# Performance work log

Hardware: AMD Instinct MI355X
Metric: run time of the kernel (lower is better)

The kernel has to match this reference:

```python
import jax, jax.numpy as jnp
import numpy as np

L, D, K = 1024, 256, 1
B, N = 16, 4096
EPS = 1e-5
NEG = -1e9


def _leaky(v):
    return jnp.where(v >= 0, v, 0.2 * v)


def setup_inputs() -> dict:
    key = jax.random.key(0)
    ks = jax.random.split(key, 16)
    s = 0.02
    x = jax.random.normal(ks[0], (B, N, L), dtype=jnp.float32)
    mask = jax.random.randint(ks[1], (B, N), 0, 2, dtype=jnp.int32)
    # guarantee >=1 valid patch per slide
    mask = mask.at[:, 0].set(1)
    return {
        "x": x,
        "mask": mask,
        # attention MLP: Linear(L,D) -> BN(D) -> LeakyReLU -> Linear(D,D) -> LeakyReLU -> Linear(D,K)
        "W1": jax.random.normal(ks[2], (L, D), jnp.float32) * s,
        "b1": jnp.zeros((D,), jnp.float32),
        "bn_gamma": jnp.ones((D,), jnp.float32),
        "bn_beta": jnp.zeros((D,), jnp.float32),
        "bn_mean": jax.random.normal(ks[3], (D,), jnp.float32) * 0.1,
        "bn_var": jax.random.uniform(ks[4], (D,), jnp.float32, 0.5, 1.5),
        "W2": jax.random.normal(ks[5], (D, D), jnp.float32) * s,
        "b2": jnp.zeros((D,), jnp.float32),
        "W3": jax.random.normal(ks[6], (D, K), jnp.float32) * s,
        "b3": jnp.zeros((K,), jnp.float32),
        # classifier MLP: Linear(L,D) -> ReLU -> Linear(D,D) -> ReLU -> Linear(D,2)
        "C1": jax.random.normal(ks[7], (L, D), jnp.float32) * s,
        "c1": jnp.zeros((D,), jnp.float32),
        "C2": jax.random.normal(ks[8], (D, D), jnp.float32) * s,
        "c2": jnp.zeros((D,), jnp.float32),
        "C3": jax.random.normal(ks[9], (D, 2), jnp.float32) * s,
        "c3": jnp.zeros((2,), jnp.float32),
    }


def reference(x, mask, W1, b1, bn_gamma, bn_beta, bn_mean, bn_var,
              W2, b2, W3, b3, C1, c1, C2, c2, C3, c3):
    # attention scores for every patch (batched; invalid patches masked later)
    h = jnp.einsum('bnl,ld->bnd', x, W1) + b1                     # [B,N,D]
    h = (h - bn_mean) * jax.lax.rsqrt(bn_var + EPS) * bn_gamma + bn_beta  # eval-mode BN
    h = _leaky(h)
    h = _leaky(jnp.einsum('bnd,de->bne', h, W2) + b2)             # [B,N,D]
    scores = (jnp.einsum('bnd,dk->bnk', h, W3) + b3)[..., 0]      # [B,N] (K=1)
    # masked softmax over patches == softmax over gathered valid patches
    valid = mask.astype(bool)
    A = jax.nn.softmax(jnp.where(valid, scores, NEG), axis=1)     # [B,N]
    M = jnp.einsum('bn,bnl->bl', A, x)                            # [B,L] attention pool
    # classifier
    z = jax.nn.relu(M @ C1 + c1)
    z = jax.nn.relu(z @ C2 + c2)
    logits = z @ C3 + c3                                          # [B,2]
    Y_prob = jax.nn.softmax(logits, axis=1)
    Y_hat = jnp.argmax(Y_prob, axis=1)
    return Y_prob, Y_hat
```

## Files before the change

### kernel.cpp

```cpp
#include <hip/hip_runtime.h>

#define BB 16
#define NN 4096
#define LL 1024
#define DD 256
#define MTOT (BB*NN)
#define EPSV 1e-5f
#define NEGV -1e9f

typedef float f32x4_t __attribute__((ext_vector_type(4)));
typedef short bf16x8_t __attribute__((ext_vector_type(8)));

#define MFMA16(a, b, c) __builtin_amdgcn_mfma_f32_16x16x32_bf16((a), (b), (c), 0, 0, 0)

__device__ __forceinline__ ushort f2bf(float f) {
    unsigned u = __builtin_bit_cast(unsigned, f);
    u += 0x7fffu + ((u >> 16) & 1u);
    return (ushort)(u >> 16);
}
__device__ __forceinline__ float bf2f(ushort u) {
    unsigned v = ((unsigned)u) << 16;
    return __builtin_bit_cast(float, v);
}
__device__ __forceinline__ void split1(float f, ushort& hi, ushort& lo) {
    hi = f2bf(f);
    lo = f2bf(f - bf2f(hi));
}
__device__ __forceinline__ float leaky(float v) { return v >= 0.f ? v : 0.2f * v; }

__global__ __launch_bounds__(256) void prep_split_w1(const float* __restrict__ W1,
                                                     ushort* __restrict__ thi,
                                                     ushort* __restrict__ tlo) {
    int idx = blockIdx.x * 256 + threadIdx.x;
    int k = idx >> 8, d = idx & 255;
    float v = W1[idx];
    ushort hi, lo; split1(v, hi, lo);
    thi[d * 1024 + k] = hi;
    tlo[d * 1024 + k] = lo;
}

__global__ __launch_bounds__(256) void prep_split_w2(const float* __restrict__ W2,
                                                     ushort* __restrict__ thi,
                                                     ushort* __restrict__ tlo) {
    int idx = blockIdx.x * 256 + threadIdx.x;
    int k = idx >> 8, d = idx & 255;
    float v = W2[idx];
    ushort hi, lo; split1(v, hi, lo);
    thi[d * 256 + k] = hi;
    tlo[d * 256 + k] = lo;
}

__global__ __launch_bounds__(256) void prep_bn(const float* __restrict__ g,
                                               const float* __restrict__ beta,
                                               const float* __restrict__ mean,
                                               const float* __restrict__ var,
                                               float* __restrict__ scale,
                                               float* __restrict__ shift) {
    int d = threadIdx.x;
    float s = g[d] * rsqrtf(var[d] + EPSV);
    scale[d] = s;
    shift[d] = beta[d] - mean[d] * s;
}

__global__ __launch_bounds__(256) void zero_scores(float* __restrict__ s) {
    s[blockIdx.x * 256 + threadIdx.x] = 0.f;
}

__global__ __launch_bounds__(256, 2) void gemm1_kernel(const float* __restrict__ x,
                                                       const ushort* __restrict__ Bhi,
                                                       const ushort* __restrict__ Blo,
                                                       const float* __restrict__ b1,
                                                       const float* __restrict__ scale,
                                                       const float* __restrict__ shift,
                                                       float* __restrict__ h) {
    __shared__ ushort sAhi[128 * 64];
    __shared__ ushort sAlo[128 * 64];
    __shared__ ushort sBhi[128 * 64];
    __shared__ ushort sBlo[128 * 64];

    const int tid = threadIdx.x;
    const int lane = tid & 63;
    const int wave = tid >> 6;
    const int wm = wave >> 1, wn = wave & 1;
    const int mblk = blockIdx.x, nblk = blockIdx.y;

    f32x4_t acc[4][4] = {};

    const int ar = tid >> 4;
    const int ac = (tid & 15) * 4;
    const int brr = tid >> 3;
    const int bcc = (tid & 7) * 8;

    const size_t xbase = (size_t)(mblk * 128) * 1024;
    const int dbase = nblk * 128;

    for (int k0 = 0; k0 < 1024; k0 += 64) {
        #pragma unroll
        for (int s = 0; s < 8; ++s) {
            int r = s * 16 + ar;
            float4 v = *reinterpret_cast<const float4*>(x + xbase + (size_t)r * 1024 + k0 + ac);
            int uo = r * 64 + (ac ^ ((r & 7) << 3));
            ushort4 hi, lo;
            split1(v.x, hi.x, lo.x); split1(v.y, hi.y, lo.y);
            split1(v.z, hi.z, lo.z); split1(v.w, hi.w, lo.w);
            *reinterpret_cast<ushort4*>(&sAhi[uo]) = hi;
            *reinterpret_cast<ushort4*>(&sAlo[uo]) = lo;
        }
        #pragma unroll
        for (int s = 0; s < 4; ++s) {
            int r = s * 32 + brr;
            size_t gsrc = (size_t)(dbase + r) * 1024 + k0 + bcc;
            int uo = r * 64 + (bcc ^ ((r & 7) << 3));
            *reinterpret_cast<uint4*>(&sBhi[uo]) = *reinterpret_cast<const uint4*>(Bhi + gsrc);
            *reinterpret_cast<uint4*>(&sBlo[uo]) = *reinterpret_cast<const uint4*>(Blo + gsrc);
        }
        __syncthreads();
        #pragma unroll
        for (int s = 0; s < 2; ++s) {
            const int kb = s * 32 + (lane >> 4) * 8;
            bf16x8_t aHi[4], aLo[4], bHi[4], bLo[4];
            #pragma unroll
            for (int i = 0; i < 4; ++i) {
                int row = wm * 64 + i * 16 + (lane & 15);
                int uo = row * 64 + (kb ^ ((row & 7) << 3));
                aHi[i] = *reinterpret_cast<const bf16x8_t*>(&sAhi[uo]);
                aLo[i] = *reinterpret_cast<const bf16x8_t*>(&sAlo[uo]);
            }
            #pragma unroll
            for (int j = 0; j < 4; ++j) {
                int col = wn * 64 + j * 16 + (lane & 15);
                int uo = col * 64 + (kb ^ ((col & 7) << 3));
                bHi[j] = *reinterpret_cast<const bf16x8_t*>(&sBhi[uo]);
                bLo[j] = *reinterpret_cast<const bf16x8_t*>(&sBlo[uo]);
            }
            #pragma unroll
            for (int i = 0; i < 4; ++i)
                #pragma unroll
                for (int j = 0; j < 4; ++j) {
                    acc[i][j] = MFMA16(aHi[i], bHi[j], acc[i][j]);
                    acc[i][j] = MFMA16(aHi[i], bLo[j], acc[i][j]);
                    acc[i][j] = MFMA16(aLo[i], bHi[j], acc[i][j]);
                }
        }
        __syncthreads();
    }
    #pragma unroll
    for (int j = 0; j < 4; ++j) {
        int col = dbase + wn * 64 + j * 16 + (lane & 15);
        float bj = b1[col], sc = scale[col], sh = shift[col];
        #pragma unroll
        for (int i = 0; i < 4; ++i) {
            int row0 = mblk * 128 + wm * 64 + i * 16 + ((lane >> 4) << 2);
            #pragma unroll
            for (int r = 0; r < 4; ++r) {
                float v = acc[i][j][r] + bj;
                v = v * sc + sh;
                h[(size_t)(row0 + r) * 256 + col] = leaky(v);
            }
        }
    }
}

__global__ __launch_bounds__(256, 2) void gemm2_kernel(const float* __restrict__ h,
                                                       const ushort* __restrict__ Bhi,
                                                       const ushort* __restrict__ Blo,
                                                       const float* __restrict__ b2,
                                                       const float* __restrict__ W3,
                                                       float* __restrict__ scores) {
    __shared__ ushort sAhi[128 * 64];
    __shared__ ushort sAlo[128 * 64];
    __shared__ ushort sBhi[128 * 64];
    __shared__ ushort sBlo[128 * 64];

    const int tid = threadIdx.x;
    const int lane = tid & 63;
    const int wave = tid >> 6;
    const int wm = wave >> 1, wn = wave & 1;
    const int mblk = blockIdx.x, nblk = blockIdx.y;

    f32x4_t acc[4][4] = {};

    const int ar = tid >> 4;
    const int ac = (tid & 15) * 4;
    const int brr = tid >> 3;
    const int bcc = (tid & 7) * 8;

    const size_t hbase = (size_t)(mblk * 128) * 256;
    const int dbase = nblk * 128;

    for (int k0 = 0; k0 < 256; k0 += 64) {
        #pragma unroll
        for (int s = 0; s < 8; ++s) {
            int r = s * 16 + ar;
            float4 v = *reinterpret_cast<const float4*>(h + hbase + (size_t)r * 256 + k0 + ac);
            int uo = r * 64 + (ac ^ ((r & 7) << 3));
            ushort4 hi, lo;
            split1(v.x, hi.x, lo.x); split1(v.y, hi.y, lo.y);
            split1(v.z, hi.z, lo.z); split1(v.w, hi.w, lo.w);
            *reinterpret_cast<ushort4*>(&sAhi[uo]) = hi;
            *reinterpret_cast<ushort4*>(&sAlo[uo]) = lo;
        }
        #pragma unroll
        for (int s = 0; s < 4; ++s) {
            int r = s * 32 + brr;
            size_t gsrc = (size_t)(dbase + r) * 256 + k0 + bcc;
            int uo = r * 64 + (bcc ^ ((r & 7) << 3));
            *reinterpret_cast<uint4*>(&sBhi[uo]) = *reinterpret_cast<const uint4*>(Bhi + gsrc);
            *reinterpret_cast<uint4*>(&sBlo[uo]) = *reinterpret_cast<const uint4*>(Blo + gsrc);
        }
        __syncthreads();
        #pragma unroll
        for (int s = 0; s < 2; ++s) {
            const int kb = s * 32 + (lane >> 4) * 8;
            bf16x8_t aHi[4], aLo[4], bHi[4], bLo[4];
            #pragma unroll
            for (int i = 0; i < 4; ++i) {
                int row = wm * 64 + i * 16 + (lane & 15);
                int uo = row * 64 + (kb ^ ((row & 7) << 3));
                aHi[i] = *reinterpret_cast<const bf16x8_t*>(&sAhi[uo]);
                aLo[i] = *reinterpret_cast<const bf16x8_t*>(&sAlo[uo]);
            }
            #pragma unroll
            for (int j = 0; j < 4; ++j) {
                int col = wn * 64 + j * 16 + (lane & 15);
                int uo = col * 64 + (kb ^ ((col & 7) << 3));
                bHi[j] = *reinterpret_cast<const bf16x8_t*>(&sBhi[uo]);
                bLo[j] = *reinterpret_cast<const bf16x8_t*>(&sBlo[uo]);
            }
            #pragma unroll
            for (int i = 0; i < 4; ++i)
                #pragma unroll
                for (int j = 0; j < 4; ++j) {
                    acc[i][j] = MFMA16(aHi[i], bHi[j], acc[i][j]);
                    acc[i][j] = MFMA16(aHi[i], bLo[j], acc[i][j]);
                    acc[i][j] = MFMA16(aLo[i], bHi[j], acc[i][j]);
                }
        }
        __syncthreads();
    }
    #pragma unroll
    for (int i = 0; i < 4; ++i) {
        float rowsum[4] = {0.f, 0.f, 0.f, 0.f};
        #pragma unroll
        for (int j = 0; j < 4; ++j) {
            int col = dbase + wn * 64 + j * 16 + (lane & 15);
            float bj = b2[col];
            float w3v = W3[col];
            #pragma unroll
            for (int r = 0; r < 4; ++r) {
                float v = leaky(acc[i][j][r] + bj);
                rowsum[r] += v * w3v;
            }
        }
        int row0 = mblk * 128 + wm * 64 + i * 16 + ((lane >> 4) << 2);
        #pragma unroll
        for (int r = 0; r < 4; ++r) {
            float s = rowsum[r];
            s += __shfl_xor(s, 1);
            s += __shfl_xor(s, 2);
            s += __shfl_xor(s, 4);
            s += __shfl_xor(s, 8);
            if ((lane & 15) == 0) atomicAdd(&scores[row0 + r], s);
        }
    }
}

__global__ __launch_bounds__(256) void softmax_kernel(const float* __restrict__ scores,
                                                      const int* __restrict__ mask,
                                                      const float* __restrict__ b3,
                                                      float* __restrict__ A,
                                                      float* __restrict__ Mz) {
    int b = blockIdx.x, tid = threadIdx.x;
    __shared__ float red[8];
    float loc[16];
    float mx = -3.4e38f;
    float b3v = b3[0];
    #pragma unroll
    for (int j = 0; j < 16; ++j) {
        int n = j * 256 + tid;
        float s = scores[b * 4096 + n] + b3v;
        if (mask[b * 4096 + n] == 0) s = NEGV;
        loc[j] = s;
        mx = fmaxf(mx, s);
    }
    #pragma unroll
    for (int o = 1; o < 64; o <<= 1) mx = fmaxf(mx, __shfl_xor(mx, o));
    if ((tid & 63) == 0) red[tid >> 6] = mx;
    __syncthreads();
    mx = fmaxf(fmaxf(red[0], red[1]), fmaxf(red[2], red[3]));
    float sum = 0.f;
    #pragma unroll
    for (int j = 0; j < 16; ++j) {
        loc[j] = expf(loc[j] - mx);
        sum += loc[j];
    }
    #pragma unroll
    for (int o = 1; o < 64; o <<= 1) sum += __shfl_xor(sum, o);
    if ((tid & 63) == 0) red[4 + (tid >> 6)] = sum;
    __syncthreads();
    sum = red[4] + red[5] + red[6] + red[7];
    float inv = 1.0f / sum;
    #pragma unroll
    for (int j = 0; j < 16; ++j) A[b * 4096 + j * 256 + tid] = loc[j] * inv;
    #pragma unroll
    for (int j = 0; j < 4; ++j) Mz[b * 1024 + j * 256 + tid] = 0.f;
}

__global__ __launch_bounds__(256) void pool_kernel(const float* __restrict__ x,
                                                   const float* __restrict__ A,
                                                   float* __restrict__ M) {
    int b = blockIdx.x, s = blockIdx.y, tid = threadIdx.x;
    __shared__ float sA[64];
    if (tid < 64) sA[tid] = A[b * 4096 + s * 64 + tid];
    __syncthreads();
    float4 acc = {0.f, 0.f, 0.f, 0.f};
    const float* xp = x + ((size_t)b * 4096 + (size_t)s * 64) * 1024 + tid * 4;
    #pragma unroll 4
    for (int n = 0; n < 64; ++n) {
        float a = sA[n];
        float4 v = *reinterpret_cast<const float4*>(xp + (size_t)n * 1024);
        acc.x += a * v.x; acc.y += a * v.y; acc.z += a * v.z; acc.w += a * v.w;
    }
    float* mp = M + b * 1024 + tid * 4;
    atomicAdd(mp + 0, acc.x);
    atomicAdd(mp + 1, acc.y);
    atomicAdd(mp + 2, acc.z);
    atomicAdd(mp + 3, acc.w);
}

__global__ __launch_bounds__(256) void classifier_kernel(const float* __restrict__ M,
                                                         const float* __restrict__ C1,
                                                         const float* __restrict__ c1,
                                                         const float* __restrict__ C2,
                                                         const float* __restrict__ c2,
                                                         const float* __restrict__ C3,
                                                         const float* __restrict__ c3,
                                                         float* __restrict__ out) {
    int b = blockIdx.x, tid = threadIdx.x;
    __shared__ float sM[1024];
    __shared__ float sZ[256];
    __shared__ float sZ2[256];
    __shared__ float sLg[2];
    #pragma unroll
    for (int j = 0; j < 4; ++j) sM[j * 256 + tid] = M[b * 1024 + j * 256 + tid];
    __syncthreads();
    float a = c1[tid];
    for (int l = 0; l < 1024; ++l) a += sM[l] * C1[l * 256 + tid];
    sZ[tid] = a > 0.f ? a : 0.f;
    __syncthreads();
    float a2 = c2[tid];
    for (int l = 0; l < 256; ++l) a2 += sZ[l] * C2[l * 256 + tid];
    sZ2[tid] = a2 > 0.f ? a2 : 0.f;
    __syncthreads();
    if (tid < 2) {
        float lg = c3[tid];
        for (int l = 0; l < 256; ++l) lg += sZ2[l] * C3[l * 2 + tid];
        sLg[tid] = lg;
    }
    __syncthreads();
    if (tid == 0) {
        float l0 = sLg[0], l1 = sLg[1];
        float mxv = fmaxf(l0, l1);
        float e0 = expf(l0 - mxv), e1 = expf(l1 - mxv);
        float sm = e0 + e1;
        out[b * 2 + 0] = e0 / sm;
        out[b * 2 + 1] = e1 / sm;
        out[32 + b] = (l1 > l0) ? 1.f : 0.f;
    }
}

extern "C" void kernel_launch(void* const* d_in, const int* in_sizes, int n_in,
                              void* d_out, int out_size, void* d_ws, size_t ws_size,
                              hipStream_t stream) {
    const float* x        = (const float*)d_in[0];
    const int*   mask     = (const int*)d_in[1];
    const float* W1       = (const float*)d_in[2];
    const float* b1       = (const float*)d_in[3];
    const float* bn_gamma = (const float*)d_in[4];
    const float* bn_beta  = (const float*)d_in[5];
    const float* bn_mean  = (const float*)d_in[6];
    const float* bn_var   = (const float*)d_in[7];
    const float* W2       = (const float*)d_in[8];
    const float* b2       = (const float*)d_in[9];
    const float* W3       = (const float*)d_in[10];
    const float* b3       = (const float*)d_in[11];
    const float* C1       = (const float*)d_in[12];
    const float* c1       = (const float*)d_in[13];
    const float* C2       = (const float*)d_in[14];
    const float* c2       = (const float*)d_in[15];
    const float* C3       = (const float*)d_in[16];
    const float* c3       = (const float*)d_in[17];
    float* out = (float*)d_out;

    ushort* w1t_hi  = (ushort*)d_ws;
    ushort* w1t_lo  = w1t_hi + 262144;
    ushort* w2t_hi  = w1t_lo + 262144;
    ushort* w2t_lo  = w2t_hi + 65536;
    float*  bn_scale = (float*)(w2t_lo + 65536);
    float*  bn_shift = bn_scale + 256;
    float*  scores   = bn_shift + 256;
    float*  attnA    = scores + 65536;
    float*  Mpool    = attnA + 65536;
    float*  h        = Mpool + 16384;

    prep_split_w1<<<1024, 256, 0, stream>>>(W1, w1t_hi, w1t_lo);
    prep_split_w2<<<256, 256, 0, stream>>>(W2, w2t_hi, w2t_lo);
    prep_bn<<<1, 256, 0, stream>>>(bn_gamma, bn_beta, bn_mean, bn_var, bn_scale, bn_shift);
    zero_scores<<<256, 256, 0, stream>>>(scores);

    gemm1_kernel<<<dim3(512, 2), 256, 0, stream>>>(x, w1t_hi, w1t_lo, b1, bn_scale, bn_shift, h);
    gemm2_kernel<<<dim3(512, 2), 256, 0, stream>>>(h, w2t_hi, w2t_lo, b2, W3, scores);
    softmax_kernel<<<16, 256, 0, stream>>>(scores, mask, b3, attnA, Mpool);
    pool_kernel<<<dim3(16, 64), 256, 0, stream>>>(x, attnA, Mpool);
    classifier_kernel<<<16, 256, 0, stream>>>(Mpool, C1, c1, C2, c2, C3, c3, out);
}
```

Before: 637.9 us.

## Pre-tile weights and h into interleaved hi/lo bf16 tiles with direct LDS loads

```diff
diff --git a/kernel.cpp b/kernel.cpp
--- a/kernel.cpp
+++ b/kernel.cpp
@@ -1,12 +1,8 @@
 #include <hip/hip_runtime.h>
 
-#define BB 16
-#define NN 4096
-#define LL 1024
-#define DD 256
-#define MTOT (BB*NN)
 #define EPSV 1e-5f
 #define NEGV -1e9f
+#define XRS(r) (((r)&7)<<3)
 
 typedef float f32x4_t __attribute__((ext_vector_type(4)));
 typedef short bf16x8_t __attribute__((ext_vector_type(8)));
@@ -28,234 +24,202 @@
 }
 __device__ __forceinline__ float leaky(float v) { return v >= 0.f ? v : 0.2f * v; }
 
-__global__ __launch_bounds__(256) void prep_split_w1(const float* __restrict__ W1,
-                                                     ushort* __restrict__ thi,
-                                                     ushort* __restrict__ tlo) {
-    int idx = blockIdx.x * 256 + threadIdx.x;
-    int k = idx >> 8, d = idx & 255;
-    float v = W1[idx];
-    ushort hi, lo; split1(v, hi, lo);
-    thi[d * 1024 + k] = hi;
-    tlo[d * 1024 + k] = lo;
-}
-
-__global__ __launch_bounds__(256) void prep_split_w2(const float* __restrict__ W2,
-                                                     ushort* __restrict__ thi,
-                                                     ushort* __restrict__ tlo) {
-    int idx = blockIdx.x * 256 + threadIdx.x;
-    int k = idx >> 8, d = idx & 255;
-    float v = W2[idx];
-    ushort hi, lo; split1(v, hi, lo);
-    thi[d * 256 + k] = hi;
-    tlo[d * 256 + k] = lo;
-}
-
-__global__ __launch_bounds__(256) void prep_bn(const float* __restrict__ g,
-                                               const float* __restrict__ beta,
-                                               const float* __restrict__ mean,
-                                               const float* __restrict__ var,
-                                               float* __restrict__ scale,
-                                               float* __restrict__ shift) {
-    int d = threadIdx.x;
-    float s = g[d] * rsqrtf(var[d] + EPSV);
-    scale[d] = s;
-    shift[d] = beta[d] - mean[d] * s;
-}
-
-__global__ __launch_bounds__(256) void zero_scores(float* __restrict__ s) {
-    s[blockIdx.x * 256 + threadIdx.x] = 0.f;
-}
-
-__global__ __launch_bounds__(256, 2) void gemm1_kernel(const float* __restrict__ x,
-                                                       const ushort* __restrict__ Bhi,
-                                                       const ushort* __restrict__ Blo,
+__device__ __forceinline__ void g2lds16(void* lds, const void* g) {
+    __builtin_amdgcn_global_load_lds(
+        (const __attribute__((address_space(1))) void*)g,
+        (__attribute__((address_space(3))) void*)lds, 16, 0, 0);
+}
+
+__global__ __launch_bounds__(256) void prep_all(const float* __restrict__ W1,
+                                                const float* __restrict__ W2,
+                                                const float* __restrict__ g,
+                                                const float* __restrict__ be,
+                                                const float* __restrict__ mn,
+                                                const float* __restrict__ vr,
+                                                ushort* __restrict__ w1t,
+                                                ushort* __restrict__ w2t,
+                                                float* __restrict__ bnsc,
+                                                float* __restrict__ bnsh,
+                                                float* __restrict__ scores) {
+    int blk = blockIdx.x, tid = threadIdx.x;
+    if (blk < 1024) {
+        int idx = blk * 256 + tid;
+        int k = idx >> 8, d = idx & 255;
+        ushort hi, lo; split1(W1[idx], hi, lo);
+        int u = (k >> 5) * 16384 + d * 64 + ((k & 31) ^ XRS(d));
+        w1t[u] = hi; w1t[u ^ 32] = lo;
+    } else if (blk < 1280) {
+        int idx = (blk - 1024) * 256 + tid;
+        int k = idx >> 8, e = idx & 255;
+        ushort hi, lo; split1(W2[idx], hi, lo);
+        int u = (k >> 5) * 16384 + e * 64 + ((k & 31) ^ XRS(e));
+        w2t[u] = hi; w2t[u ^ 32] = lo;
+    } else if (blk == 1280) {
+        float s = g[tid] * rsqrtf(vr[tid] + EPSV);
+        bnsc[tid] = s; bnsh[tid] = be[tid] - mn[tid] * s;
+    } else {
+        int idx = (blk - 1281) * 256 + tid;
+        scores[idx] = 0.f;
+    }
+}
+
+__global__ __launch_bounds__(256, 4) void gemm1_kernel(const float* __restrict__ x,
+                                                       const ushort* __restrict__ w1t,
                                                        const float* __restrict__ b1,
-                                                       const float* __restrict__ scale,
-                                                       const float* __restrict__ shift,
-                                                       float* __restrict__ h) {
-    __shared__ ushort sAhi[128 * 64];
-    __shared__ ushort sAlo[128 * 64];
-    __shared__ ushort sBhi[128 * 64];
-    __shared__ ushort sBlo[128 * 64];
-
-    const int tid = threadIdx.x;
-    const int lane = tid & 63;
-    const int wave = tid >> 6;
+                                                       const float* __restrict__ bnsc,
+                                                       const float* __restrict__ bnsh,
+                                                       ushort* __restrict__ hsp) {
+    __shared__ ushort sA[128 * 64];
+    __shared__ ushort sB[128 * 64];
+
+    const int bid = blockIdx.x;
+    const int swz = (bid & 7) * 128 + (bid >> 3);
+    const int mblk = swz >> 1, nblk = swz & 1;
+    const int tid = threadIdx.x, lane = tid & 63, wave = tid >> 6;
     const int wm = wave >> 1, wn = wave & 1;
-    const int mblk = blockIdx.x, nblk = blockIdx.y;
 
     f32x4_t acc[4][4] = {};
 
-    const int ar = tid >> 4;
-    const int ac = (tid & 15) * 4;
-    const int brr = tid >> 3;
-    const int bcc = (tid & 7) * 8;
-
+    const int arow = tid >> 3;
+    const int acol = (tid & 7) * 4;
     const size_t xbase = (size_t)(mblk * 128) * 1024;
-    const int dbase = nblk * 128;
-
-    for (int k0 = 0; k0 < 1024; k0 += 64) {
-        #pragma unroll
-        for (int s = 0; s < 8; ++s) {
-            int r = s * 16 + ar;
-            float4 v = *reinterpret_cast<const float4*>(x + xbase + (size_t)r * 1024 + k0 + ac);
-            int uo = r * 64 + (ac ^ ((r & 7) << 3));
+    const ushort* wbase = w1t + nblk * 8192;
+
+    for (int k0 = 0; k0 < 32; ++k0) {
+        const ushort* bs = wbase + (size_t)k0 * 16384;
+        #pragma unroll
+        for (int i = 0; i < 4; ++i)
+            g2lds16(&sB[i * 2048 + tid * 8], bs + i * 2048 + tid * 8);
+        #pragma unroll
+        for (int s = 0; s < 4; ++s) {
+            int r = s * 32 + arow;
+            float4 v = *reinterpret_cast<const float4*>(x + xbase + (size_t)r * 1024 + k0 * 32 + acol);
             ushort4 hi, lo;
             split1(v.x, hi.x, lo.x); split1(v.y, hi.y, lo.y);
             split1(v.z, hi.z, lo.z); split1(v.w, hi.w, lo.w);
-            *reinterpret_cast<ushort4*>(&sAhi[uo]) = hi;
-            *reinterpret_cast<ushort4*>(&sAlo[uo]) = lo;
-        }
-        #pragma unroll
-        for (int s = 0; s < 4; ++s) {
-            int r = s * 32 + brr;
-            size_t gsrc = (size_t)(dbase + r) * 1024 + k0 + bcc;
-            int uo = r * 64 + (bcc ^ ((r & 7) << 3));
-            *reinterpret_cast<uint4*>(&sBhi[uo]) = *reinterpret_cast<const uint4*>(Bhi + gsrc);
-            *reinterpret_cast<uint4*>(&sBlo[uo]) = *reinterpret_cast<const uint4*>(Blo + gsrc);
+            int u = r * 64 + (acol ^ XRS(r));
+            *reinterpret_cast<ushort4*>(&sA[u]) = hi;
+            *reinterpret_cast<ushort4*>(&sA[u ^ 32]) = lo;
         }
         __syncthreads();
-        #pragma unroll
-        for (int s = 0; s < 2; ++s) {
-            const int kb = s * 32 + (lane >> 4) * 8;
-            bf16x8_t aHi[4], aLo[4], bHi[4], bLo[4];
+        {
+            const int g8 = (lane >> 4) * 8;
+            bf16x8_t aH[4], aL[4], bH[4], bL[4];
             #pragma unroll
             for (int i = 0; i < 4; ++i) {
                 int row = wm * 64 + i * 16 + (lane & 15);
-                int uo = row * 64 + (kb ^ ((row & 7) << 3));
-                aHi[i] = *reinterpret_cast<const bf16x8_t*>(&sAhi[uo]);
-                aLo[i] = *reinterpret_cast<const bf16x8_t*>(&sAlo[uo]);
+                int u = row * 64 + (g8 ^ XRS(row));
+                aH[i] = *reinterpret_cast<const bf16x8_t*>(&sA[u]);
+                aL[i] = *reinterpret_cast<const bf16x8_t*>(&sA[u ^ 32]);
             }
             #pragma unroll
             for (int j = 0; j < 4; ++j) {
                 int col = wn * 64 + j * 16 + (lane & 15);
-                int uo = col * 64 + (kb ^ ((col & 7) << 3));
-                bHi[j] = *reinterpret_cast<const bf16x8_t*>(&sBhi[uo]);
-                bLo[j] = *reinterpret_cast<const bf16x8_t*>(&sBlo[uo]);
+                int u = col * 64 + (g8 ^ XRS(col));
+                bH[j] = *reinterpret_cast<const bf16x8_t*>(&sB[u]);
+                bL[j] = *reinterpret_cast<const bf16x8_t*>(&sB[u ^ 32]);
             }
             #pragma unroll
             for (int i = 0; i < 4; ++i)
                 #pragma unroll
                 for (int j = 0; j < 4; ++j) {
-                    acc[i][j] = MFMA16(aHi[i], bHi[j], acc[i][j]);
-                    acc[i][j] = MFMA16(aHi[i], bLo[j], acc[i][j]);
-                    acc[i][j] = MFMA16(aLo[i], bHi[j], acc[i][j]);
+                    acc[i][j] = MFMA16(aH[i], bH[j], acc[i][j]);
+                    acc[i][j] = MFMA16(aH[i], bL[j], acc[i][j]);
+                    acc[i][j] = MFMA16(aL[i], bH[j], acc[i][j]);
                 }
         }
         __syncthreads();
     }
     #pragma unroll
     for (int j = 0; j < 4; ++j) {
-        int col = dbase + wn * 64 + j * 16 + (lane & 15);
-        float bj = b1[col], sc = scale[col], sh = shift[col];
+        int colg = nblk * 128 + wn * 64 + j * 16 + (lane & 15);
+        float bj = b1[colg], sc = bnsc[colg], sh = bnsh[colg];
+        int cl = colg & 31;
+        size_t tbase = ((size_t)mblk * 8 + (colg >> 5)) * 8192;
         #pragma unroll
         for (int i = 0; i < 4; ++i) {
-            int row0 = mblk * 128 + wm * 64 + i * 16 + ((lane >> 4) << 2);
+            int rl0 = wm * 64 + i * 16 + ((lane >> 4) << 2);
             #pragma unroll
             for (int r = 0; r < 4; ++r) {
-                float v = acc[i][j][r] + bj;
-                v = v * sc + sh;
-                h[(size_t)(row0 + r) * 256 + col] = leaky(v);
-            }
-        }
-    }
-}
-
-__global__ __launch_bounds__(256, 2) void gemm2_kernel(const float* __restrict__ h,
-                                                       const ushort* __restrict__ Bhi,
-                                                       const ushort* __restrict__ Blo,
+                int rl = rl0 + r;
+                float v = leaky((acc[i][j][r] + bj) * sc + sh);
+                ushort hi, lo; split1(v, hi, lo);
+                int u = rl * 64 + (cl ^ XRS(rl));
+                hsp[tbase + u] = hi;
+                hsp[tbase + (u ^ 32)] = lo;
+            }
+        }
+    }
+}
+
+__global__ __launch_bounds__(256, 4) void gemm2_kernel(const ushort* __restrict__ hsp,
+                                                       const ushort* __restrict__ w2t,
                                                        const float* __restrict__ b2,
                                                        const float* __restrict__ W3,
                                                        float* __restrict__ scores) {
-    __shared__ ushort sAhi[128 * 64];
-    __shared__ ushort sAlo[128 * 64];
-    __shared__ ushort sBhi[128 * 64];
-    __shared__ ushort sBlo[128 * 64];
-
-    const int tid = threadIdx.x;
-    const int lane = tid & 63;
-    const int wave = tid >> 6;
+    __shared__ ushort sA[128 * 64];
+    __shared__ ushort sB[128 * 64];
+
+    const int bid = blockIdx.x;
+    const int swz = (bid & 7) * 128 + (bid >> 3);
+    const int mblk = swz >> 1, nblk = swz & 1;
+    const int tid = threadIdx.x, lane = tid & 63, wave = tid >> 6;
     const int wm = wave >> 1, wn = wave & 1;
-    const int mblk = blockIdx.x, nblk = blockIdx.y;
 
     f32x4_t acc[4][4] = {};
 
-    const int ar = tid >> 4;
-    const int ac = (tid & 15) * 4;
-    const int brr = tid >> 3;
-    const int bcc = (tid & 7) * 8;
-
-    const size_t hbase = (size_t)(mblk * 128) * 256;
-    const int dbase = nblk * 128;
-
-    for (int k0 = 0; k0 < 256; k0 += 64) {
-        #pragma unroll
-        for (int s = 0; s < 8; ++s) {
-            int r = s * 16 + ar;
-            float4 v = *reinterpret_cast<const float4*>(h + hbase + (size_t)r * 256 + k0 + ac);
-            int uo = r * 64 + (ac ^ ((r & 7) << 3));
-            ushort4 hi, lo;
-            split1(v.x, hi.x, lo.x); split1(v.y, hi.y, lo.y);
-            split1(v.z, hi.z, lo.z); split1(v.w, hi.w, lo.w);
-            *reinterpret_cast<ushort4*>(&sAhi[uo]) = hi;
-            *reinterpret_cast<ushort4*>(&sAlo[uo]) = lo;
-        }
-        #pragma unroll
-        for (int s = 0; s < 4; ++s) {
-            int r = s * 32 + brr;
-            size_t gsrc = (size_t)(dbase + r) * 256 + k0 + bcc;
-            int uo = r * 64 + (bcc ^ ((r & 7) << 3));
-            *reinterpret_cast<uint4*>(&sBhi[uo]) = *reinterpret_cast<const uint4*>(Bhi + gsrc);
-            *reinterpret_cast<uint4*>(&sBlo[uo]) = *reinterpret_cast<const uint4*>(Blo + gsrc);
+    for (int k0 = 0; k0 < 8; ++k0) {
+        const ushort* as = hsp + ((size_t)mblk * 8 + k0) * 8192;
+        const ushort* bs = w2t + (size_t)k0 * 16384 + nblk * 8192;
+        #pragma unroll
+        for (int i = 0; i < 4; ++i) {
+            g2lds16(&sA[i * 2048 + tid * 8], as + i * 2048 + tid * 8);
+            g2lds16(&sB[i * 2048 + tid * 8], bs + i * 2048 + tid * 8);
         }
         __syncthreads();
-        #pragma unroll
-        for (int s = 0; s < 2; ++s) {
-            const int kb = s * 32 + (lane >> 4) * 8;
-            bf16x8_t aHi[4], aLo[4], bHi[4], bLo[4];
+        {
+            const int g8 = (lane >> 4) * 8;
+            bf16x8_t aH[4], aL[4], bH[4], bL[4];
             #pragma unroll
             for (int i = 0; i < 4; ++i) {
                 int row = wm * 64 + i * 16 + (lane & 15);
-                int uo = row * 64 + (kb ^ ((row & 7) << 3));
-                aHi[i] = *reinterpret_cast<const bf16x8_t*>(&sAhi[uo]);
-                aLo[i] = *reinterpret_cast<const bf16x8_t*>(&sAlo[uo]);
+                int u = row * 64 + (g8 ^ XRS(row));
+                aH[i] = *reinterpret_cast<const bf16x8_t*>(&sA[u]);
+                aL[i] = *reinterpret_cast<const bf16x8_t*>(&sA[u ^ 32]);
             }
             #pragma unroll
             for (int j = 0; j < 4; ++j) {
                 int col = wn * 64 + j * 16 + (lane & 15);
-                int uo = col * 64 + (kb ^ ((col & 7) << 3));
-                bHi[j] = *reinterpret_cast<const bf16x8_t*>(&sBhi[uo]);
-                bLo[j] = *reinterpret_cast<const bf16x8_t*>(&sBlo[uo]);
+                int u = col * 64 + (g8 ^ XRS(col));
+                bH[j] = *reinterpret_cast<const bf16x8_t*>(&sB[u]);
+                bL[j] = *reinterpret_cast<const bf16x8_t*>(&sB[u ^ 32]);
             }
             #pragma unroll
             for (int i = 0; i < 4; ++i)
                 #pragma unroll
                 for (int j = 0; j < 4; ++j) {
-                    acc[i][j] = MFMA16(aHi[i], bHi[j], acc[i][j]);
-                    acc[i][j] = MFMA16(aHi[i], bLo[j], acc[i][j]);
-                    acc[i][j] = MFMA16(aLo[i], bHi[j], acc[i][j]);
+                    acc[i][j] = MFMA16(aH[i], bH[j], acc[i][j]);
+                    acc[i][j] = MFMA16(aH[i], bL[j], acc[i][j]);
+                    acc[i][j] = MFMA16(aL[i], bH[j], acc[i][j]);
                 }
         }
         __syncthreads();
     }
     #pragma unroll
     for (int i = 0; i < 4; ++i) {
-        float rowsum[4] = {0.f, 0.f, 0.f, 0.f};
+        float rs[4] = {0.f, 0.f, 0.f, 0.f};
         #pragma unroll
         for (int j = 0; j < 4; ++j) {
-            int col = dbase + wn * 64 + j * 16 + (lane & 15);
-            float bj = b2[col];
-            float w3v = W3[col];
-            #pragma unroll
-            for (int r = 0; r < 4; ++r) {
-                float v = leaky(acc[i][j][r] + bj);
-                rowsum[r] += v * w3v;
-            }
+            int colg = nblk * 128 + wn * 64 + j * 16 + (lane & 15);
+            float bj = b2[colg], w3v = W3[colg];
+            #pragma unroll
+            for (int r = 0; r < 4; ++r)
+                rs[r] += leaky(acc[i][j][r] + bj) * w3v;
         }
         int row0 = mblk * 128 + wm * 64 + i * 16 + ((lane >> 4) << 2);
         #pragma unroll
         for (int r = 0; r < 4; ++r) {
-            float s = rowsum[r];
+            float s = rs[r];
             s += __shfl_xor(s, 1);
             s += __shfl_xor(s, 2);
             s += __shfl_xor(s, 4);
@@ -310,13 +274,13 @@
                                                    const float* __restrict__ A,
                                                    float* __restrict__ M) {
     int b = blockIdx.x, s = blockIdx.y, tid = threadIdx.x;
-    __shared__ float sA[64];
-    if (tid < 64) sA[tid] = A[b * 4096 + s * 64 + tid];
+    __shared__ float sA[128];
+    if (tid < 128) sA[tid] = A[b * 4096 + s * 128 + tid];
     __syncthreads();
     float4 acc = {0.f, 0.f, 0.f, 0.f};
-    const float* xp = x + ((size_t)b * 4096 + (size_t)s * 64) * 1024 + tid * 4;
-    #pragma unroll 4
-    for (int n = 0; n < 64; ++n) {
+    const float* xp = x + ((size_t)b * 4096 + (size_t)s * 128) * 1024 + tid * 4;
+    #pragma unroll 8
+    for (int n = 0; n < 128; ++n) {
         float a = sA[n];
         float4 v = *reinterpret_cast<const float4*>(xp + (size_t)n * 1024);
         acc.x += a * v.x; acc.y += a * v.y; acc.z += a * v.z; acc.w += a * v.w;
@@ -392,25 +356,20 @@
     const float* c3       = (const float*)d_in[17];
     float* out = (float*)d_out;
 
-    ushort* w1t_hi  = (ushort*)d_ws;
-    ushort* w1t_lo  = w1t_hi + 262144;
-    ushort* w2t_hi  = w1t_lo + 262144;
-    ushort* w2t_lo  = w2t_hi + 65536;
-    float*  bn_scale = (float*)(w2t_lo + 65536);
-    float*  bn_shift = bn_scale + 256;
-    float*  scores   = bn_shift + 256;
-    float*  attnA    = scores + 65536;
-    float*  Mpool    = attnA + 65536;
-    float*  h        = Mpool + 16384;
-
-    prep_split_w1<<<1024, 256, 0, stream>>>(W1, w1t_hi, w1t_lo);
-    prep_split_w2<<<256, 256, 0, stream>>>(W2, w2t_hi, w2t_lo);
-    prep_bn<<<1, 256, 0, stream>>>(bn_gamma, bn_beta, bn_mean, bn_var, bn_scale, bn_shift);
-    zero_scores<<<256, 256, 0, stream>>>(scores);
-
-    gemm1_kernel<<<dim3(512, 2), 256, 0, stream>>>(x, w1t_hi, w1t_lo, b1, bn_scale, bn_shift, h);
-    gemm2_kernel<<<dim3(512, 2), 256, 0, stream>>>(h, w2t_hi, w2t_lo, b2, W3, scores);
+    ushort* w1t   = (ushort*)d_ws;
+    ushort* w2t   = w1t + 524288;
+    float*  bnsc  = (float*)(w2t + 131072);
+    float*  bnsh  = bnsc + 256;
+    float*  scores = bnsh + 256;
+    float*  attnA  = scores + 65536;
+    float*  Mpool  = attnA + 65536;
+    ushort* hsp    = (ushort*)(Mpool + 16384);
+
+    prep_all<<<1537, 256, 0, stream>>>(W1, W2, bn_gamma, bn_beta, bn_mean, bn_var,
+                                       w1t, w2t, bnsc, bnsh, scores);
+    gemm1_kernel<<<1024, 256, 0, stream>>>(x, w1t, b1, bnsc, bnsh, hsp);
+    gemm2_kernel<<<1024, 256, 0, stream>>>(hsp, w2t, b2, W3, scores);
     softmax_kernel<<<16, 256, 0, stream>>>(scores, mask, b3, attnA, Mpool);
-    pool_kernel<<<dim3(16, 64), 256, 0, stream>>>(x, attnA, Mpool);
+    pool_kernel<<<dim3(16, 32), 256, 0, stream>>>(x, attnA, Mpool);
     classifier_kernel<<<16, 256, 0, stream>>>(Mpool, C1, c1, C2, c2, C3, c3, out);
 }
```

After: 626.5 us. About the same (-1.8%).
